# Kernel tuning notes

Hardware: AMD Instinct MI355X
Metric: run time of the kernel (lower is better)

Reference implementation:

```python
import jax, jax.numpy as jnp
import numpy as np

DATA_SIZE = 16
WIDTH = 128
BATCH = 4096
T0 = 0.0
DT = 0.1
T1 = 1.0
N_STEPS = 10  # round((T1 - T0) / DT), ConstantStepSize + dt0=0.1


def setup_inputs() -> dict:
    key = jax.random.key(0)
    ks = jax.random.split(key, 7)

    def init(k, shape):
        fan_in = shape[-1]
        return jax.random.normal(k, shape, jnp.float32) / np.float32(np.sqrt(fan_in))

    return {
        "y": jax.random.normal(ks[0], (BATCH, DATA_SIZE), jnp.float32),
        "W1": init(ks[1], (WIDTH, DATA_SIZE + 1)),
        "b1": jax.random.normal(ks[2], (WIDTH,), jnp.float32) * 0.01,
        "W2": init(ks[3], (WIDTH, WIDTH)),
        "b2": jax.random.normal(ks[4], (WIDTH,), jnp.float32) * 0.01,
        "W3": init(ks[5], (DATA_SIZE, WIDTH)),
        "b3": jax.random.normal(ks[6], (DATA_SIZE,), jnp.float32) * 0.01,
    }


def reference(y, W1, b1, W2, b2, W3, b3):
    """ContinuousNormalizingFlow.transform_and_log_det with exact_logp=True,
    ReversibleHeun solver, ConstantStepSize, vmapped over a batch of samples.
    Returns (transformed_y [B, d], delta_log_likelihood [B])."""
    d = y.shape[-1]

    def drift(t, yv):  # yv: [d] -> [d]   (MLPFunc.__call__)
        x = jnp.concatenate([yv, t[None]])  # [d+1]
        h = jax.nn.silu(W1 @ x + b1)
        h = jax.nn.silu(W2 @ h + b2)
        return W3 @ h + b3

    def drift_and_trace(t, yv):  # exact_logp_wrapper per sample
        f, vjp_fn = jax.vjp(lambda z: drift(t, z), yv)
        (dfdy,) = jax.vmap(vjp_fn)(jnp.eye(d, dtype=yv.dtype))  # [d, d]
        return f, jnp.trace(dfdy)

    vf = jax.vmap(drift_and_trace, in_axes=(None, 0))  # -> ([B, d], [B])

    dt = jnp.float32(DT)
    t0 = jnp.float32(T0)
    l0 = jnp.zeros(y.shape[0], y.dtype)

    # ReversibleHeun: auxiliary state yhat starts at y0, vf evaluated once at t0.
    fy0, fl0 = vf(t0, y)
    state = (y, l0, y, l0, fy0, fl0)

    def step(state, i):
        yc, lc, yh, lh, fy, fl = state
        t1 = t0 + (i.astype(jnp.float32) + 1.0) * dt
        yh1 = 2.0 * yc - yh + dt * fy
        lh1 = 2.0 * lc - lh + dt * fl
        fy1, fl1 = vf(t1, yh1)
        y1 = yc + 0.5 * dt * (fy + fy1)
        l1 = lc + 0.5 * dt * (fl + fl1)
        return (y1, l1, yh1, lh1, fy1, fl1), None

    state, _ = jax.lax.scan(step, state, jnp.arange(N_STEPS))
    return state[0], state[1]
```

## Files before the change

### kernel.cpp

```cpp
#include <hip/hip_runtime.h>
#include <stdint.h>

typedef _Float16 f16x8 __attribute__((ext_vector_type(8)));
typedef float f32x4 __attribute__((ext_vector_type(4)));

#define MFMA16(a, b, c) __builtin_amdgcn_mfma_f32_16x16x32_f16(a, b, c, 0, 0, 0)

__global__ void cnf_prep(const float* __restrict__ W1, const float* __restrict__ W2,
                         const float* __restrict__ W3, float* __restrict__ G) {
    int idx = blockIdx.x * 256 + threadIdx.x;
    int i = idx >> 7, k = idx & 127;
    float m = 0.f;
#pragma unroll
    for (int mm = 0; mm < 16; ++mm) m += W1[i * 17 + mm] * W3[mm * 128 + k];
    G[idx] = m * W2[k * 128 + i];
}

__launch_bounds__(256)
__global__ void cnf_main(const float* __restrict__ y,
                         const float* __restrict__ W1, const float* __restrict__ b1,
                         const float* __restrict__ W2, const float* __restrict__ b2,
                         const float* __restrict__ W3, const float* __restrict__ b3,
                         const float* __restrict__ G, float* __restrict__ out) {
    __shared__ _Float16 H1[128 * 16];
    __shared__ _Float16 H2[128 * 16];
    __shared__ _Float16 S2[128 * 16];
    __shared__ float YIN[16 * 20];
    __shared__ float TR[4 * 16];

    const int tid = threadIdx.x;
    const int w   = tid >> 6;
    const int l   = tid & 63;
    const int col = l & 15;
    const int g4  = l >> 4;
    const int sbase = blockIdx.x * 16;

    f16x8 W1f[2], W2f[2][4], Gf[2][4];
    float b1r[2][4], b2r[2][4];
#pragma unroll
    for (int m = 0; m < 2; ++m) {
        const int row = w * 32 + m * 16 + col;
        f16x8 a;
#pragma unroll
        for (int j = 0; j < 8; ++j) {
            int k = g4 * 8 + j;
            a[j] = (_Float16)(k < 17 ? W1[row * 17 + k] : 0.f);
        }
        W1f[m] = a;
#pragma unroll
        for (int ks = 0; ks < 4; ++ks) {
            f16x8 aw, ag;
#pragma unroll
            for (int j = 0; j < 8; ++j) {
                int k = ks * 32 + g4 * 8 + j;
                aw[j] = (_Float16)W2[row * 128 + k];
                ag[j] = (_Float16)G[row * 128 + k];
            }
            W2f[m][ks] = aw;
            Gf[m][ks]  = ag;
        }
#pragma unroll
        for (int r = 0; r < 4; ++r) {
            int rr = w * 32 + m * 16 + g4 * 4 + r;
            b1r[m][r] = b1[rr];
            b2r[m][r] = b2[rr];
        }
    }

    f16x8 W3f[4];
    float b3r[4];
    f32x4 yc{}, yh{}, fy{};
    float lc = 0.f, lh = 0.f, fl = 0.f;
    if (w == 0) {
#pragma unroll
        for (int ks = 0; ks < 4; ++ks) {
            f16x8 a;
#pragma unroll
            for (int j = 0; j < 8; ++j)
                a[j] = (_Float16)W3[col * 128 + ks * 32 + g4 * 8 + j];
            W3f[ks] = a;
        }
#pragma unroll
        for (int r = 0; r < 4; ++r) b3r[r] = b3[g4 * 4 + r];
#pragma unroll
        for (int r = 0; r < 4; ++r) {
            float v = y[(sbase + col) * 16 + g4 * 4 + r];
            yc[r] = v;
            yh[r] = v;
            YIN[col * 20 + g4 * 4 + r] = v;
        }
    }

    for (int e = 0; e <= 10; ++e) {
        __syncthreads();
        const float t = 0.1f * (float)e;

        f16x8 Xf;
#pragma unroll
        for (int j = 0; j < 8; ++j) {
            int k = g4 * 8 + j;
            float v;
            if (k < 16) v = YIN[col * 20 + k];
            else        v = (k == 16) ? t : 0.f;
            Xf[j] = (_Float16)v;
        }

        float s1v[2][4];
#pragma unroll
        for (int m = 0; m < 2; ++m) {
            f32x4 c = {b1r[m][0], b1r[m][1], b1r[m][2], b1r[m][3]};
            c = MFMA16(W1f[m], Xf, c);
            union { _Float16 h[4]; uint32_t u[2]; } pk;
#pragma unroll
            for (int r = 0; r < 4; ++r) {
                float z   = c[r];
                float sig = 1.f / (1.f + __expf(-z));
                float h   = z * sig;
                s1v[m][r] = sig + h * (1.f - sig);
                pk.h[r]   = (_Float16)h;
            }
            int rowb = w * 32 + m * 16 + g4 * 4;
            uint32_t* p = (uint32_t*)&H1[(rowb >> 3) * 128 + col * 8 + (rowb & 7)];
            p[0] = pk.u[0];
            p[1] = pk.u[1];
        }
        __syncthreads();

        f16x8 Bf[4];
#pragma unroll
        for (int ks = 0; ks < 4; ++ks)
            Bf[ks] = *(const f16x8*)&H1[(g4 + ks * 4) * 128 + col * 8];
#pragma unroll
        for (int m = 0; m < 2; ++m) {
            f32x4 c = {b2r[m][0], b2r[m][1], b2r[m][2], b2r[m][3]};
#pragma unroll
            for (int ks = 0; ks < 4; ++ks) c = MFMA16(W2f[m][ks], Bf[ks], c);
            union { _Float16 h[4]; uint32_t u[2]; } pk, ps;
#pragma unroll
            for (int r = 0; r < 4; ++r) {
                float z   = c[r];
                float sig = 1.f / (1.f + __expf(-z));
                float h   = z * sig;
                pk.h[r] = (_Float16)h;
                ps.h[r] = (_Float16)(sig + h * (1.f - sig));
            }
            int rowb = w * 32 + m * 16 + g4 * 4;
            int idx  = (rowb >> 3) * 128 + col * 8 + (rowb & 7);
            uint32_t* p2 = (uint32_t*)&H2[idx];
            p2[0] = pk.u[0]; p2[1] = pk.u[1];
            uint32_t* p3 = (uint32_t*)&S2[idx];
            p3[0] = ps.u[0]; p3[1] = ps.u[1];
        }
        __syncthreads();

#pragma unroll
        for (int ks = 0; ks < 4; ++ks)
            Bf[ks] = *(const f16x8*)&S2[(g4 + ks * 4) * 128 + col * 8];
        float p = 0.f;
#pragma unroll
        for (int m = 0; m < 2; ++m) {
            f32x4 c{};
#pragma unroll
            for (int ks = 0; ks < 4; ++ks) c = MFMA16(Gf[m][ks], Bf[ks], c);
#pragma unroll
            for (int r = 0; r < 4; ++r) p += s1v[m][r] * c[r];
        }
        p += __shfl_xor(p, 16);
        p += __shfl_xor(p, 32);
        if (l < 16) TR[w * 16 + l] = p;

        f32x4 fn{};
        if (w == 0) {
            f16x8 Hf[4];
#pragma unroll
            for (int ks = 0; ks < 4; ++ks)
                Hf[ks] = *(const f16x8*)&H2[(g4 + ks * 4) * 128 + col * 8];
            f32x4 c = {b3r[0], b3r[1], b3r[2], b3r[3]};
#pragma unroll
            for (int ks = 0; ks < 4; ++ks) c = MFMA16(W3f[ks], Hf[ks], c);
            fn = c;
        }
        __syncthreads();

        if (w == 0) {
            float fln = TR[col] + TR[16 + col] + TR[32 + col] + TR[48 + col];
            if (e == 0) {
                fy = fn; fl = fln;
            } else {
#pragma unroll
                for (int r = 0; r < 4; ++r) yc[r] += 0.05f * (fy[r] + fn[r]);
                lc += 0.05f * (fl + fln);
                fy = fn; fl = fln;
            }
            if (e < 10) {
                f32x4 yhn;
#pragma unroll
                for (int r = 0; r < 4; ++r) {
                    yhn[r] = 2.f * yc[r] - yh[r] + 0.1f * fy[r];
                    YIN[col * 20 + g4 * 4 + r] = yhn[r];
                }
                yh = yhn;
                lh = 2.f * lc - lh + 0.1f * fl;
            }
        }
    }

    if (w == 0) {
#pragma unroll
        for (int r = 0; r < 4; ++r)
            out[(sbase + col) * 16 + g4 * 4 + r] = yc[r];
        if (l < 16) out[4096 * 16 + sbase + l] = lc;
    }
}

extern "C" void kernel_launch(void* const* d_in, const int* in_sizes, int n_in,
                              void* d_out, int out_size, void* d_ws, size_t ws_size,
                              hipStream_t stream) {
    const float* y  = (const float*)d_in[0];
    const float* W1 = (const float*)d_in[1];
    const float* b1 = (const float*)d_in[2];
    const float* W2 = (const float*)d_in[3];
    const float* b2 = (const float*)d_in[4];
    const float* W3 = (const float*)d_in[5];
    const float* b3 = (const float*)d_in[6];
    float* out = (float*)d_out;
    float* G   = (float*)d_ws;

    cnf_prep<<<64, 256, 0, stream>>>(W1, W2, W3, G);
    cnf_main<<<256, 256, 0, stream>>>(y, W1, b1, W2, b2, W3, b3, G, out);
}
```

Before: 33.50 us.

## Replicate output layer per wave to drop per-step barriers and shared state

Every wave now computes the W3 output layer and keeps the ODE state in registers. The next-step input is built with cross-lane shuffles instead of a shared-memory round trip, which removes two of the four barriers per step. The log-det trace is accumulated per wave with trapezoid weights and reduced across waves only once at the end. G is stored as fp16 by the prep kernel, weights are loaded with float4, and the MFMA accumulation chains are split into two independent accumulators to shorten dependencies. The cost is redundant W3 MFMAs in all four waves and higher register pressure (launch bounds set to 1).

```diff
diff --git a/kernel.cpp b/kernel.cpp
--- a/kernel.cpp
+++ b/kernel.cpp
@@ -6,27 +6,32 @@
 
 #define MFMA16(a, b, c) __builtin_amdgcn_mfma_f32_16x16x32_f16(a, b, c, 0, 0, 0)
 
+static __device__ __forceinline__ uint32_t pkh(float a, float b) {
+    union { _Float16 h[2]; uint32_t u; } v;
+    v.h[0] = (_Float16)a; v.h[1] = (_Float16)b;
+    return v.u;
+}
+
 __global__ void cnf_prep(const float* __restrict__ W1, const float* __restrict__ W2,
-                         const float* __restrict__ W3, float* __restrict__ G) {
+                         const float* __restrict__ W3, _Float16* __restrict__ Gh) {
     int idx = blockIdx.x * 256 + threadIdx.x;
     int i = idx >> 7, k = idx & 127;
     float m = 0.f;
 #pragma unroll
     for (int mm = 0; mm < 16; ++mm) m += W1[i * 17 + mm] * W3[mm * 128 + k];
-    G[idx] = m * W2[k * 128 + i];
-}
-
-__launch_bounds__(256)
+    Gh[idx] = (_Float16)(m * W2[k * 128 + i]);
+}
+
+__launch_bounds__(256, 1)
 __global__ void cnf_main(const float* __restrict__ y,
                          const float* __restrict__ W1, const float* __restrict__ b1,
                          const float* __restrict__ W2, const float* __restrict__ b2,
                          const float* __restrict__ W3, const float* __restrict__ b3,
-                         const float* __restrict__ G, float* __restrict__ out) {
+                         const _Float16* __restrict__ Gh, float* __restrict__ out) {
     __shared__ _Float16 H1[128 * 16];
     __shared__ _Float16 H2[128 * 16];
     __shared__ _Float16 S2[128 * 16];
-    __shared__ float YIN[16 * 20];
-    __shared__ float TR[4 * 16];
+    __shared__ float PS[4 * 16];
 
     const int tid = threadIdx.x;
     const int w   = tid >> 6;
@@ -35,8 +40,8 @@
     const int g4  = l >> 4;
     const int sbase = blockIdx.x * 16;
 
-    f16x8 W1f[2], W2f[2][4], Gf[2][4];
-    float b1r[2][4], b2r[2][4];
+    f16x8 W1f[2], W2f[2][4], Gf[2][4], W3f[4];
+    float b1r[2][4], b2r[2][4], b3r[4];
 #pragma unroll
     for (int m = 0; m < 2; ++m) {
         const int row = w * 32 + m * 16 + col;
@@ -49,15 +54,12 @@
         W1f[m] = a;
 #pragma unroll
         for (int ks = 0; ks < 4; ++ks) {
-            f16x8 aw, ag;
-#pragma unroll
-            for (int j = 0; j < 8; ++j) {
-                int k = ks * 32 + g4 * 8 + j;
-                aw[j] = (_Float16)W2[row * 128 + k];
-                ag[j] = (_Float16)G[row * 128 + k];
-            }
+            const float4* pw = (const float4*)&W2[row * 128 + ks * 32 + g4 * 8];
+            float4 w0 = pw[0], w1 = pw[1];
+            f16x8 aw = {(_Float16)w0.x, (_Float16)w0.y, (_Float16)w0.z, (_Float16)w0.w,
+                        (_Float16)w1.x, (_Float16)w1.y, (_Float16)w1.z, (_Float16)w1.w};
             W2f[m][ks] = aw;
-            Gf[m][ks]  = ag;
+            Gf[m][ks]  = *(const f16x8*)&Gh[row * 128 + ks * 32 + g4 * 8];
         }
 #pragma unroll
         for (int r = 0; r < 4; ++r) {
@@ -66,63 +68,59 @@
             b2r[m][r] = b2[rr];
         }
     }
-
-    f16x8 W3f[4];
-    float b3r[4];
-    f32x4 yc{}, yh{}, fy{};
-    float lc = 0.f, lh = 0.f, fl = 0.f;
-    if (w == 0) {
-#pragma unroll
-        for (int ks = 0; ks < 4; ++ks) {
-            f16x8 a;
-#pragma unroll
-            for (int j = 0; j < 8; ++j)
-                a[j] = (_Float16)W3[col * 128 + ks * 32 + g4 * 8 + j];
-            W3f[ks] = a;
-        }
-#pragma unroll
-        for (int r = 0; r < 4; ++r) b3r[r] = b3[g4 * 4 + r];
-#pragma unroll
-        for (int r = 0; r < 4; ++r) {
-            float v = y[(sbase + col) * 16 + g4 * 4 + r];
-            yc[r] = v;
-            yh[r] = v;
-            YIN[col * 20 + g4 * 4 + r] = v;
-        }
-    }
+#pragma unroll
+    for (int ks = 0; ks < 4; ++ks) {
+        const float4* pw = (const float4*)&W3[col * 128 + ks * 32 + g4 * 8];
+        float4 w0 = pw[0], w1 = pw[1];
+        f16x8 a = {(_Float16)w0.x, (_Float16)w0.y, (_Float16)w0.z, (_Float16)w0.w,
+                   (_Float16)w1.x, (_Float16)w1.y, (_Float16)w1.z, (_Float16)w1.w};
+        W3f[ks] = a;
+    }
+#pragma unroll
+    for (int r = 0; r < 4; ++r) b3r[r] = b3[g4 * 4 + r];
+
+    f32x4 yc, yh, fy, xsrc;
+#pragma unroll
+    for (int r = 0; r < 4; ++r) {
+        float v = y[(sbase + col) * 16 + g4 * 4 + r];
+        yc[r] = v; yh[r] = v; xsrc[r] = v;
+    }
+    float plsum = 0.f;
 
     for (int e = 0; e <= 10; ++e) {
-        __syncthreads();
         const float t = 0.1f * (float)e;
 
-        f16x8 Xf;
-#pragma unroll
-        for (int j = 0; j < 8; ++j) {
-            int k = g4 * 8 + j;
-            float v;
-            if (k < 16) v = YIN[col * 20 + k];
-            else        v = (k == 16) ? t : 0.f;
-            Xf[j] = (_Float16)v;
-        }
+        uint32_t u0 = pkh(xsrc[0], xsrc[1]);
+        uint32_t u1 = pkh(xsrc[2], xsrc[3]);
+        int s0 = (g4 * 32 + col) & 63;
+        uint32_t xw0 = (uint32_t)__shfl((int)u0, s0);
+        uint32_t xw1 = (uint32_t)__shfl((int)u1, s0);
+        uint32_t xw2 = (uint32_t)__shfl((int)u0, (s0 + 16) & 63);
+        uint32_t xw3 = (uint32_t)__shfl((int)u1, (s0 + 16) & 63);
+        if (g4 == 2) { xw0 = pkh(t, 0.f); xw1 = 0u; xw2 = 0u; xw3 = 0u; }
+        if (g4 == 3) { xw0 = 0u; xw1 = 0u; xw2 = 0u; xw3 = 0u; }
+        union { uint32_t u[4]; f16x8 f; } xu;
+        xu.u[0] = xw0; xu.u[1] = xw1; xu.u[2] = xw2; xu.u[3] = xw3;
+        f16x8 Xf = xu.f;
 
         float s1v[2][4];
 #pragma unroll
         for (int m = 0; m < 2; ++m) {
             f32x4 c = {b1r[m][0], b1r[m][1], b1r[m][2], b1r[m][3]};
             c = MFMA16(W1f[m], Xf, c);
-            union { _Float16 h[4]; uint32_t u[2]; } pk;
-#pragma unroll
-            for (int r = 0; r < 4; ++r) {
-                float z   = c[r];
-                float sig = 1.f / (1.f + __expf(-z));
-                float h   = z * sig;
-                s1v[m][r] = sig + h * (1.f - sig);
-                pk.h[r]   = (_Float16)h;
+            uint32_t pk0, pk1;
+            {
+                float z0 = c[0], z1 = c[1], z2 = c[2], z3 = c[3];
+                float g0 = 1.f / (1.f + __expf(-z0)), g1 = 1.f / (1.f + __expf(-z1));
+                float g2 = 1.f / (1.f + __expf(-z2)), g3 = 1.f / (1.f + __expf(-z3));
+                float h0 = z0 * g0, h1 = z1 * g1, h2 = z2 * g2, h3 = z3 * g3;
+                s1v[m][0] = g0 + h0 * (1.f - g0); s1v[m][1] = g1 + h1 * (1.f - g1);
+                s1v[m][2] = g2 + h2 * (1.f - g2); s1v[m][3] = g3 + h3 * (1.f - g3);
+                pk0 = pkh(h0, h1); pk1 = pkh(h2, h3);
             }
             int rowb = w * 32 + m * 16 + g4 * 4;
             uint32_t* p = (uint32_t*)&H1[(rowb >> 3) * 128 + col * 8 + (rowb & 7)];
-            p[0] = pk.u[0];
-            p[1] = pk.u[1];
+            p[0] = pk0; p[1] = pk1;
         }
         __syncthreads();
 
@@ -132,84 +130,89 @@
             Bf[ks] = *(const f16x8*)&H1[(g4 + ks * 4) * 128 + col * 8];
 #pragma unroll
         for (int m = 0; m < 2; ++m) {
-            f32x4 c = {b2r[m][0], b2r[m][1], b2r[m][2], b2r[m][3]};
-#pragma unroll
-            for (int ks = 0; ks < 4; ++ks) c = MFMA16(W2f[m][ks], Bf[ks], c);
-            union { _Float16 h[4]; uint32_t u[2]; } pk, ps;
-#pragma unroll
-            for (int r = 0; r < 4; ++r) {
-                float z   = c[r];
-                float sig = 1.f / (1.f + __expf(-z));
-                float h   = z * sig;
-                pk.h[r] = (_Float16)h;
-                ps.h[r] = (_Float16)(sig + h * (1.f - sig));
+            f32x4 ca = {b2r[m][0], b2r[m][1], b2r[m][2], b2r[m][3]};
+            f32x4 cb = {0.f, 0.f, 0.f, 0.f};
+            ca = MFMA16(W2f[m][0], Bf[0], ca);
+            cb = MFMA16(W2f[m][1], Bf[1], cb);
+            ca = MFMA16(W2f[m][2], Bf[2], ca);
+            cb = MFMA16(W2f[m][3], Bf[3], cb);
+            uint32_t h0u, h1u, s0u, s1u;
+            {
+                float z0 = ca[0] + cb[0], z1 = ca[1] + cb[1];
+                float z2 = ca[2] + cb[2], z3 = ca[3] + cb[3];
+                float g0 = 1.f / (1.f + __expf(-z0)), g1 = 1.f / (1.f + __expf(-z1));
+                float g2 = 1.f / (1.f + __expf(-z2)), g3 = 1.f / (1.f + __expf(-z3));
+                float h0 = z0 * g0, h1 = z1 * g1, h2 = z2 * g2, h3 = z3 * g3;
+                h0u = pkh(h0, h1); h1u = pkh(h2, h3);
+                s0u = pkh(g0 + h0 * (1.f - g0), g1 + h1 * (1.f - g1));
+                s1u = pkh(g2 + h2 * (1.f - g2), g3 + h3 * (1.f - g3));
             }
             int rowb = w * 32 + m * 16 + g4 * 4;
             int idx  = (rowb >> 3) * 128 + col * 8 + (rowb & 7);
             uint32_t* p2 = (uint32_t*)&H2[idx];
-            p2[0] = pk.u[0]; p2[1] = pk.u[1];
+            p2[0] = h0u; p2[1] = h1u;
             uint32_t* p3 = (uint32_t*)&S2[idx];
-            p3[0] = ps.u[0]; p3[1] = ps.u[1];
+            p3[0] = s0u; p3[1] = s1u;
         }
         __syncthreads();
 
-#pragma unroll
-        for (int ks = 0; ks < 4; ++ks)
-            Bf[ks] = *(const f16x8*)&S2[(g4 + ks * 4) * 128 + col * 8];
+        f16x8 Sf[4], Hf[4];
+#pragma unroll
+        for (int ks = 0; ks < 4; ++ks) {
+            Sf[ks] = *(const f16x8*)&S2[(g4 + ks * 4) * 128 + col * 8];
+            Hf[ks] = *(const f16x8*)&H2[(g4 + ks * 4) * 128 + col * 8];
+        }
         float p = 0.f;
 #pragma unroll
         for (int m = 0; m < 2; ++m) {
-            f32x4 c{};
-#pragma unroll
-            for (int ks = 0; ks < 4; ++ks) c = MFMA16(Gf[m][ks], Bf[ks], c);
-#pragma unroll
-            for (int r = 0; r < 4; ++r) p += s1v[m][r] * c[r];
+            f32x4 c0 = {0.f, 0.f, 0.f, 0.f}, c1 = {0.f, 0.f, 0.f, 0.f};
+            c0 = MFMA16(Gf[m][0], Sf[0], c0);
+            c1 = MFMA16(Gf[m][1], Sf[1], c1);
+            c0 = MFMA16(Gf[m][2], Sf[2], c0);
+            c1 = MFMA16(Gf[m][3], Sf[3], c1);
+#pragma unroll
+            for (int r = 0; r < 4; ++r) p += s1v[m][r] * (c0[r] + c1[r]);
         }
         p += __shfl_xor(p, 16);
         p += __shfl_xor(p, 32);
-        if (l < 16) TR[w * 16 + l] = p;
-
-        f32x4 fn{};
-        if (w == 0) {
-            f16x8 Hf[4];
-#pragma unroll
-            for (int ks = 0; ks < 4; ++ks)
-                Hf[ks] = *(const f16x8*)&H2[(g4 + ks * 4) * 128 + col * 8];
-            f32x4 c = {b3r[0], b3r[1], b3r[2], b3r[3]};
-#pragma unroll
-            for (int ks = 0; ks < 4; ++ks) c = MFMA16(W3f[ks], Hf[ks], c);
-            fn = c;
-        }
-        __syncthreads();
-
-        if (w == 0) {
-            float fln = TR[col] + TR[16 + col] + TR[32 + col] + TR[48 + col];
-            if (e == 0) {
-                fy = fn; fl = fln;
-            } else {
-#pragma unroll
-                for (int r = 0; r < 4; ++r) yc[r] += 0.05f * (fy[r] + fn[r]);
-                lc += 0.05f * (fl + fln);
-                fy = fn; fl = fln;
-            }
-            if (e < 10) {
-                f32x4 yhn;
-#pragma unroll
-                for (int r = 0; r < 4; ++r) {
-                    yhn[r] = 2.f * yc[r] - yh[r] + 0.1f * fy[r];
-                    YIN[col * 20 + g4 * 4 + r] = yhn[r];
-                }
-                yh = yhn;
-                lh = 2.f * lc - lh + 0.1f * fl;
-            }
-        }
-    }
-
+        plsum += ((e == 0 || e == 10) ? 0.05f : 0.1f) * p;
+
+        f32x4 fa = {b3r[0], b3r[1], b3r[2], b3r[3]};
+        f32x4 fb = {0.f, 0.f, 0.f, 0.f};
+        fa = MFMA16(W3f[0], Hf[0], fa);
+        fb = MFMA16(W3f[1], Hf[1], fb);
+        fa = MFMA16(W3f[2], Hf[2], fa);
+        fb = MFMA16(W3f[3], Hf[3], fb);
+
+        if (e == 0) {
+#pragma unroll
+            for (int r = 0; r < 4; ++r) fy[r] = fa[r] + fb[r];
+        } else {
+#pragma unroll
+            for (int r = 0; r < 4; ++r) {
+                float fn = fa[r] + fb[r];
+                yc[r] += 0.05f * (fy[r] + fn);
+                fy[r] = fn;
+            }
+        }
+        if (e < 10) {
+#pragma unroll
+            for (int r = 0; r < 4; ++r) {
+                float v = 2.f * yc[r] - yh[r] + 0.1f * fy[r];
+                xsrc[r] = v;
+                yh[r] = v;
+            }
+        }
+    }
+
+    if (l < 16) PS[w * 16 + l] = plsum;
+    __syncthreads();
     if (w == 0) {
 #pragma unroll
         for (int r = 0; r < 4; ++r)
             out[(sbase + col) * 16 + g4 * 4 + r] = yc[r];
-        if (l < 16) out[4096 * 16 + sbase + l] = lc;
+        if (l < 16)
+            out[4096 * 16 + sbase + l] = PS[l] + PS[16 + l] + PS[32 + l] + PS[48 + l];
     }
 }
 
@@ -224,8 +227,8 @@
     const float* W3 = (const float*)d_in[5];
     const float* b3 = (const float*)d_in[6];
     float* out = (float*)d_out;
-    float* G   = (float*)d_ws;
-
-    cnf_prep<<<64, 256, 0, stream>>>(W1, W2, W3, G);
-    cnf_main<<<256, 256, 0, stream>>>(y, W1, b1, W2, b2, W3, b3, G, out);
-}
+    _Float16* Gh = (_Float16*)d_ws;
+
+    cnf_prep<<<64, 256, 0, stream>>>(W1, W2, W3, Gh);
+    cnf_main<<<256, 256, 0, stream>>>(y, W1, b1, W2, b2, W3, b3, Gh, out);
+}
```

Result: faster. 30.36 us (-9.4%).
